# Kernel tuning notes

Hardware: AMD Instinct MI355X
Metric: run time of the kernel (lower is better)

Reference implementation:

```python
import jax, jax.numpy as jnp
import numpy as np


def setup_inputs() -> dict:
    key = jax.random.key(0)
    ks = jax.random.split(key, 6)
    B, T, D, H = 32, 2048, 1024, 1024
    s = jax.random.normal(ks[0], (1, B, D), dtype=jnp.float32)
    h = jax.random.normal(ks[1], (B, T, D), dtype=jnp.float32)
    mask = jax.random.randint(ks[2], (B, T), 0, 2, dtype=jnp.int32)
    W = jax.random.normal(ks[3], (D, H), dtype=jnp.float32) * (6.0 / (D + H)) ** 0.5
    U = jax.random.normal(ks[4], (D, H), dtype=jnp.float32) * (6.0 / (D + H)) ** 0.5
    v = jax.random.normal(ks[5], (H, 1), dtype=jnp.float32) * (6.0 / (H + 1)) ** 0.5
    return {"s": s, "h": h, "mask": mask, "W": W, "U": U, "v": v}


def reference(s, h, mask, W, U, v):
    # mask-fill encoder states: zero out padded timesteps
    m = (mask != 0)[:, :, None]            # (B, T, 1)
    h = jnp.where(m, h, 0.0)               # (B, T, D)
    s_t = jnp.transpose(s, (1, 0, 2))      # (B, 1, D)
    proj_s = s_t @ W                       # (B, 1, H)
    proj_h = h @ U                         # (B, T, H)
    energy = jnp.tanh(proj_s + proj_h) @ v  # (B, T, 1)
    energy = jnp.where(m, energy, -1e9)
    score = jax.nn.softmax(energy, axis=1)  # softmax over time
    context = jnp.sum(score * h, axis=1)    # (B, D)
    return context
```

## Files before the change

### kernel.cpp

```cpp
#include <hip/hip_runtime.h>
#include <hip/hip_fp16.h>
#include <math.h>

#define BB 32
#define TT 2048
#define DD 1024
#define HH 1024
#define MM (BB*TT)

typedef _Float16 half8 __attribute__((ext_vector_type(8)));
typedef float f32x4 __attribute__((ext_vector_type(4)));

__device__ __forceinline__ float tanh_fast(float x) {
    float cx = fminf(fmaxf(x, -10.0f), 10.0f);
    float e2 = __expf(2.0f * cx);
    return (e2 - 1.0f) / (e2 + 1.0f);
}

__device__ __forceinline__ void load_lds16(const _Float16* g, _Float16* l) {
    __builtin_amdgcn_global_load_lds(
        (const __attribute__((address_space(1))) void*)g,
        (__attribute__((address_space(3))) void*)l, 16, 0, 0);
}

#define CAST_BLOCKS (MM/2)
#define UT_BLOCKS   1024
#define PS_BLOCKS   128
#define CPT_BLOCKS  32
#define TOTAL_SETUP (CAST_BLOCKS + UT_BLOCKS + PS_BLOCKS + CPT_BLOCKS)

__global__ __launch_bounds__(256)
void mega_setup_kernel(const float* __restrict__ h,
                       const int* __restrict__ mask,
                       _Float16* __restrict__ h16,
                       const float* __restrict__ U,
                       _Float16* __restrict__ Ut,
                       const float* __restrict__ s,
                       const float* __restrict__ W,
                       float* __restrict__ ps,
                       float* __restrict__ out,
                       int* __restrict__ rowlist,
                       int* __restrict__ cnts) {
    __shared__ float smem[1056];
    __shared__ int wsum[4];
    const int bid = blockIdx.x;
    const int tid = threadIdx.x;

    if (bid < CAST_BLOCKS) {
        const int row = bid * 2 + (tid >> 7);
        if (mask[row] == 0) return;
        const int c = (tid & 127) * 8;
        const long base = (long)row * DD + c;
        const float4 f0 = *(const float4*)(h + base);
        const float4 f1 = *(const float4*)(h + base + 4);
        half8 o;
        o[0] = (_Float16)f0.x; o[1] = (_Float16)f0.y;
        o[2] = (_Float16)f0.z; o[3] = (_Float16)f0.w;
        o[4] = (_Float16)f1.x; o[5] = (_Float16)f1.y;
        o[6] = (_Float16)f1.z; o[7] = (_Float16)f1.w;
        *(half8*)(h16 + base) = o;
        return;
    }

    if (bid < CAST_BLOCKS + UT_BLOCKS) {
        const int id = bid - CAST_BLOCKS;
        const int bx = id & 31, by = id >> 5;
        float (*tile)[33] = (float(*)[33])smem;
        const int tx = tid & 31, ty = tid >> 5;
#pragma unroll
        for (int j = 0; j < 4; ++j)
            tile[ty + j * 8][tx] = U[(long)(by * 32 + ty + j * 8) * HH + bx * 32 + tx];
        __syncthreads();
#pragma unroll
        for (int j = 0; j < 4; ++j)
            Ut[(long)(bx * 32 + ty + j * 8) * DD + by * 32 + tx] =
                (_Float16)tile[tx][ty + j * 8];
        return;
    }

    if (bid < CAST_BLOCKS + UT_BLOCKS + PS_BLOCKS) {
        const int id = bid - (CAST_BLOCKS + UT_BLOCKS);
        const int b = id & 31, nseg = id >> 5;
        const int n = nseg * 256 + tid;
        float* ss = smem;
#pragma unroll
        for (int j = 0; j < 4; ++j)
            ss[tid + j * 256] = s[b * DD + tid + j * 256];
        out[b * DD + n] = 0.0f;
        __syncthreads();
        float a[8];
#pragma unroll
        for (int j = 0; j < 8; ++j) a[j] = 0.f;
        for (int d = 0; d < DD; d += 8) {
#pragma unroll
            for (int j = 0; j < 8; ++j)
                a[j] += ss[d + j] * W[(long)(d + j) * HH + n];
        }
        ps[b * HH + n] = ((a[0]+a[1])+(a[2]+a[3])) + ((a[4]+a[5])+(a[6]+a[7]));
        return;
    }

    {
        const int b = bid - (CAST_BLOCKS + UT_BLOCKS + PS_BLOCKS);
        const int lane = tid & 63, w = tid >> 6;
        const int* mb = mask + b * TT;
        const int t0 = tid * 8;
        int m[8], c = 0;
#pragma unroll
        for (int j = 0; j < 8; ++j) { m[j] = (mb[t0 + j] != 0); c += m[j]; }
        int pref = c;
#pragma unroll
        for (int off = 1; off < 64; off <<= 1) {
            int nv = __shfl_up(pref, off, 64);
            if (lane >= off) pref += nv;
        }
        if (lane == 63) wsum[w] = pref;
        __syncthreads();
        int wbase = 0;
        for (int i = 0; i < w; ++i) wbase += wsum[i];
        int pos = wbase + pref - c;
#pragma unroll
        for (int j = 0; j < 8; ++j)
            if (m[j]) rowlist[b * TT + pos++] = t0 + j;
        const int total = wsum[0] + wsum[1] + wsum[2] + wsum[3];
        if (tid == 0) cnts[b] = total;
        __syncthreads();
        const int padded = ((total + 127) >> 7) << 7;
        const int lastt = (total > 0) ? rowlist[b * TT + total - 1] : 0;
        for (int ci = total + tid; ci < padded; ci += 256)
            rowlist[b * TT + ci] = lastt;
    }
}

#define Bb_K 32

__global__ __launch_bounds__(256)
void energy_gemm_kernel(const _Float16* __restrict__ h16,
                        const _Float16* __restrict__ Ut,
                        const float* __restrict__ ps,
                        const float* __restrict__ v,
                        const int* __restrict__ rowlist,
                        const int* __restrict__ cnts,
                        float* __restrict__ epart) {
    const int nt = blockIdx.x;
    const int mt = blockIdx.y;
    const int b   = mt >> 4;
    const int ci0 = (mt & 15) << 7;
    if (ci0 >= cnts[b]) return;

    __shared__ _Float16 As[2][128][32];
    __shared__ _Float16 Bs[2][128][32];
    __shared__ float ps_s[128];
    __shared__ float v_s[128];
    __shared__ int   rl[128];

    const int n0  = nt * 128;
    const int tid = threadIdx.x;
    const int wave = tid >> 6, lane = tid & 63;
    const int wm = wave >> 1, wn = wave & 1;

    if (tid < 128) {
        ps_s[tid] = ps[b * HH + n0 + tid];
        v_s[tid]  = v[n0 + tid];
        rl[tid]   = rowlist[b * TT + ci0 + tid];
    }
    __syncthreads();

    const int srow = wave * 32 + (lane >> 2);
    const int sseg = (lane & 3) * 8;
    const _Float16* gA0 = h16 + ((long)b * TT + rl[srow])      * DD + sseg;
    const _Float16* gA1 = h16 + ((long)b * TT + rl[srow + 16]) * DD + sseg;
    const _Float16* gB0 = Ut + (long)(n0 + srow) * DD + sseg;
    const _Float16* gB1 = gB0 + 16 * DD;

    f32x4 acc[4][4];
#pragma unroll
    for (int i = 0; i < 4; ++i)
#pragma unroll
        for (int j = 0; j < 4; ++j) acc[i][j] = (f32x4)0.0f;

    const int lk = (lane >> 4) * 8;
    const int lr = lane & 15;

    load_lds16(gA0, &As[0][wave * 32][0]);
    load_lds16(gA1, &As[0][wave * 32 + 16][0]);
    load_lds16(gB0, &Bs[0][wave * 32][0]);
    load_lds16(gB1, &Bs[0][wave * 32 + 16][0]);
    asm volatile("s_waitcnt vmcnt(0)" ::: "memory");
    __builtin_amdgcn_s_barrier();

#define KSTEP(CUR, NXT, KS)                                                   \
    {                                                                         \
        const int k1 = ((KS) + 1) * Bb_K;                                     \
        if (k1 < DD) {                                                        \
            load_lds16(gA0 + k1, &As[NXT][wave * 32][0]);                     \
            load_lds16(gA1 + k1, &As[NXT][wave * 32 + 16][0]);                \
            load_lds16(gB0 + k1, &Bs[NXT][wave * 32][0]);                     \
            load_lds16(gB1 + k1, &Bs[NXT][wave * 32 + 16][0]);                \
        }                                                                     \
        half8 af[4], bf[4];                                                   \
        _Pragma("unroll")                                                     \
        for (int tm = 0; tm < 4; ++tm)                                        \
            af[tm] = *(const half8*)&As[CUR][wm * 64 + tm * 16 + lr][lk];     \
        _Pragma("unroll")                                                     \
        for (int tn = 0; tn < 4; ++tn)                                        \
            bf[tn] = *(const half8*)&Bs[CUR][wn * 64 + tn * 16 + lr][lk];     \
        _Pragma("unroll")                                                     \
        for (int tm = 0; tm < 4; ++tm)                                        \
            _Pragma("unroll")                                                 \
            for (int tn = 0; tn < 4; ++tn)                                    \
                acc[tm][tn] = __builtin_amdgcn_mfma_f32_16x16x32_f16(         \
                    af[tm], bf[tn], acc[tm][tn], 0, 0, 0);                    \
        asm volatile("s_waitcnt vmcnt(0)" ::: "memory");                      \
        __builtin_amdgcn_s_barrier();                                         \
    }

#pragma unroll 1
    for (int ks = 0; ks < 32; ks += 2) {
        KSTEP(0, 1, ks);
        KSTEP(1, 0, ks + 1);
    }
#undef KSTEP

    float part[4][4];
#pragma unroll
    for (int tm = 0; tm < 4; ++tm) {
#pragma unroll
        for (int r = 0; r < 4; ++r) {
            float p = 0.f;
#pragma unroll
            for (int tn = 0; tn < 4; ++tn) {
                const int cl = wn * 64 + tn * 16 + lr;
                p += v_s[cl] * tanh_fast(acc[tm][tn][r] + ps_s[cl]);
            }
            part[tm][r] = p;
        }
    }
#pragma unroll
    for (int off = 1; off < 16; off <<= 1)
#pragma unroll
        for (int tm = 0; tm < 4; ++tm)
#pragma unroll
            for (int r = 0; r < 4; ++r)
                part[tm][r] += __shfl_xor(part[tm][r], off, 64);

    if ((lane & 15) == 0) {
        const int slot = nt * 2 + wn;
#pragma unroll
        for (int tm = 0; tm < 4; ++tm)
#pragma unroll
            for (int r = 0; r < 4; ++r) {
                const int ci = ci0 + wm * 64 + tm * 16 + (lane >> 4) * 4 + r;
                epart[(long)slot * MM + b * TT + ci] = part[tm][r];
            }
    }
}

__global__ void softmax_kernel(const float* __restrict__ epart,
                               const int* __restrict__ rowlist,
                               const int* __restrict__ cnts,
                               float* __restrict__ score) {
    const int b = blockIdx.x, tid = threadIdx.x;
    const int cnt = cnts[b];
    for (int t = tid; t < TT; t += 256) score[b * TT + t] = 0.0f;

    float e[8], mx = -1e30f;
#pragma unroll
    for (int i = 0; i < 8; ++i) {
        const int ci = i * 256 + tid;
        float sum = -1e30f;
        if (ci < cnt) {
            sum = 0.f;
#pragma unroll
            for (int p = 0; p < 16; ++p)
                sum += epart[(long)p * MM + b * TT + ci];
        }
        e[i] = sum;
        mx = fmaxf(mx, sum);
    }
#pragma unroll
    for (int off = 32; off > 0; off >>= 1) mx = fmaxf(mx, __shfl_xor(mx, off, 64));
    __shared__ float r4[4];
    if ((tid & 63) == 0) r4[tid >> 6] = mx;
    __syncthreads();
    mx = fmaxf(fmaxf(r4[0], r4[1]), fmaxf(r4[2], r4[3]));

    float tot = 0.f;
#pragma unroll
    for (int i = 0; i < 8; ++i) {
        const int ci = i * 256 + tid;
        e[i] = (ci < cnt) ? __expf(e[i] - mx) : 0.0f;
        tot += e[i];
    }
#pragma unroll
    for (int off = 32; off > 0; off >>= 1) tot += __shfl_xor(tot, off, 64);
    __shared__ float s4[4];
    if ((tid & 63) == 0) s4[tid >> 6] = tot;
    __syncthreads();
    tot = s4[0] + s4[1] + s4[2] + s4[3];
    const float inv = 1.0f / tot;
#pragma unroll
    for (int i = 0; i < 8; ++i) {
        const int ci = i * 256 + tid;
        if (ci < cnt)
            score[b * TT + rowlist[b * TT + ci]] = e[i] * inv;
    }
}

__global__ void context_kernel(const _Float16* __restrict__ h16,
                               const float* __restrict__ score,
                               float* __restrict__ out) {
    const int tc = blockIdx.x;
    const int b  = blockIdx.y;
    const int d0 = threadIdx.x * 8;
    float a[8];
#pragma unroll
    for (int j = 0; j < 8; ++j) a[j] = 0.f;
    for (int i = 0; i < 128; ++i) {
        const int t = tc * 128 + i;
        const float sc = score[(long)b * TT + t];
        if (sc != 0.0f) {
            const half8 hv = *(const half8*)(h16 + ((long)(b * TT + t)) * DD + d0);
#pragma unroll
            for (int j = 0; j < 8; ++j) a[j] += sc * (float)hv[j];
        }
    }
#pragma unroll
    for (int j = 0; j < 8; ++j) atomicAdd(&out[b * DD + d0 + j], a[j]);
}

extern "C" void kernel_launch(void* const* d_in, const int* in_sizes, int n_in,
                              void* d_out, int out_size, void* d_ws, size_t ws_size,
                              hipStream_t stream) {
    const float* s    = (const float*)d_in[0];
    const float* h    = (const float*)d_in[1];
    const int*   mask = (const int*)  d_in[2];
    const float* W    = (const float*)d_in[3];
    const float* U    = (const float*)d_in[4];
    const float* v    = (const float*)d_in[5];
    float* out = (float*)d_out;

    char* ws = (char*)d_ws;
    size_t off = 0;
    _Float16* h16 = (_Float16*)(ws + off); off += (size_t)MM * DD * 2;
    _Float16* Ut  = (_Float16*)(ws + off); off += (size_t)HH * DD * 2;
    float*    ps  = (float*)(ws + off);    off += (size_t)BB * HH * 4;
    float*    ep  = (float*)(ws + off);    off += (size_t)16 * MM * 4;
    float*    scr = (float*)(ws + off);    off += (size_t)MM * 4;
    int*      rlist = (int*)(ws + off);    off += (size_t)MM * 4;
    int*      cnts  = (int*)(ws + off);    off += 64 * 4;

    mega_setup_kernel<<<TOTAL_SETUP, 256, 0, stream>>>(h, mask, h16, U, Ut,
                                                       s, W, ps, out, rlist, cnts);
    energy_gemm_kernel<<<dim3(8, 512), 256, 0, stream>>>(h16, Ut, ps, v,
                                                         rlist, cnts, ep);
    softmax_kernel<<<BB, 256, 0, stream>>>(ep, rlist, cnts, scr);
    context_kernel<<<dim3(16, 32), 128, 0, stream>>>(h16, scr, out);
}
```

Before: 562.1 us.

## Pad LDS tiles to avoid bank conflicts and remap GEMM grid for L2 reuse

Replaces the plain [128][32] LDS tiles with flat buffers padded by 8 halves per 16-row group (520-element stride), so the half8 fragment reads hit distinct banks instead of conflicting. It also flattens the 2D grid into a 1D index that groups 8 M-tiles with all 8 N-tiles, so blocks running at the same time share h rows and U columns in L2. The padding relies on the global_load_lds write pattern lining up with the new read offsets, which is easy to get wrong.

```diff
diff --git a/kernel.cpp b/kernel.cpp
--- a/kernel.cpp
+++ b/kernel.cpp
@@ -142,14 +142,17 @@
                         const int* __restrict__ rowlist,
                         const int* __restrict__ cnts,
                         float* __restrict__ epart) {
-    const int nt = blockIdx.x;
-    const int mt = blockIdx.y;
+    const int id = blockIdx.x;
+    const int c  = id & 7;
+    const int j  = id >> 3;
+    const int nt = j & 7;
+    const int mt = c + ((j >> 3) << 3);
     const int b   = mt >> 4;
     const int ci0 = (mt & 15) << 7;
     if (ci0 >= cnts[b]) return;
 
-    __shared__ _Float16 As[2][128][32];
-    __shared__ _Float16 Bs[2][128][32];
+    __shared__ _Float16 AsF[2][4160];
+    __shared__ _Float16 BsF[2][4160];
     __shared__ float ps_s[128];
     __shared__ float v_s[128];
     __shared__ int   rl[128];
@@ -177,15 +180,15 @@
 #pragma unroll
     for (int i = 0; i < 4; ++i)
 #pragma unroll
-        for (int j = 0; j < 4; ++j) acc[i][j] = (f32x4)0.0f;
+        for (int j2 = 0; j2 < 4; ++j2) acc[i][j2] = (f32x4)0.0f;
 
     const int lk = (lane >> 4) * 8;
     const int lr = lane & 15;
 
-    load_lds16(gA0, &As[0][wave * 32][0]);
-    load_lds16(gA1, &As[0][wave * 32 + 16][0]);
-    load_lds16(gB0, &Bs[0][wave * 32][0]);
-    load_lds16(gB1, &Bs[0][wave * 32 + 16][0]);
+    load_lds16(gA0, &AsF[0][(2 * wave) * 520]);
+    load_lds16(gA1, &AsF[0][(2 * wave + 1) * 520]);
+    load_lds16(gB0, &BsF[0][(2 * wave) * 520]);
+    load_lds16(gB1, &BsF[0][(2 * wave + 1) * 520]);
     asm volatile("s_waitcnt vmcnt(0)" ::: "memory");
     __builtin_amdgcn_s_barrier();
 
@@ -193,18 +196,20 @@
     {                                                                         \
         const int k1 = ((KS) + 1) * Bb_K;                                     \
         if (k1 < DD) {                                                        \
-            load_lds16(gA0 + k1, &As[NXT][wave * 32][0]);                     \
-            load_lds16(gA1 + k1, &As[NXT][wave * 32 + 16][0]);                \
-            load_lds16(gB0 + k1, &Bs[NXT][wave * 32][0]);                     \
-            load_lds16(gB1 + k1, &Bs[NXT][wave * 32 + 16][0]);                \
+            load_lds16(gA0 + k1, &AsF[NXT][(2 * wave) * 520]);                \
+            load_lds16(gA1 + k1, &AsF[NXT][(2 * wave + 1) * 520]);            \
+            load_lds16(gB0 + k1, &BsF[NXT][(2 * wave) * 520]);                \
+            load_lds16(gB1 + k1, &BsF[NXT][(2 * wave + 1) * 520]);            \
         }                                                                     \
         half8 af[4], bf[4];                                                   \
         _Pragma("unroll")                                                     \
         for (int tm = 0; tm < 4; ++tm)                                        \
-            af[tm] = *(const half8*)&As[CUR][wm * 64 + tm * 16 + lr][lk];     \
+            af[tm] = *(const half8*)&AsF[CUR][(wm * 64 + tm * 16 + lr) * 32 + \
+                                             (wm * 4 + tm) * 8 + lk];         \
         _Pragma("unroll")                                                     \
         for (int tn = 0; tn < 4; ++tn)                                        \
-            bf[tn] = *(const half8*)&Bs[CUR][wn * 64 + tn * 16 + lr][lk];     \
+            bf[tn] = *(const half8*)&BsF[CUR][(wn * 64 + tn * 16 + lr) * 32 + \
+                                             (wn * 4 + tn) * 8 + lk];         \
         _Pragma("unroll")                                                     \
         for (int tm = 0; tm < 4; ++tm)                                        \
             _Pragma("unroll")                                                 \
@@ -352,8 +357,8 @@
 
     mega_setup_kernel<<<TOTAL_SETUP, 256, 0, stream>>>(h, mask, h16, U, Ut,
                                                        s, W, ps, out, rlist, cnts);
-    energy_gemm_kernel<<<dim3(8, 512), 256, 0, stream>>>(h16, Ut, ps, v,
-                                                         rlist, cnts, ep);
+    energy_gemm_kernel<<<4096, 256, 0, stream>>>(h16, Ut, ps, v,
+                                                 rlist, cnts, ep);
     softmax_kernel<<<BB, 256, 0, stream>>>(ep, rlist, cnts, scr);
     context_kernel<<<dim3(16, 32), 128, 0, stream>>>(h16, scr, out);
 }
```

Result: no change. 571.1 us (+1.6%).
